# Kernel tuning notes

Hardware: AMD Instinct MI355X
Metric: run time of the kernel (lower is better)

Reference implementation:

```python
import jax, jax.numpy as jnp
import numpy as np

# Surrogate-gradient spike (ActFun_adp from DH-SNN): Heaviside fwd, multi-Gaussian bwd
GAMMA, LENS, SCALE, HIGHT = 0.5, 0.5, 6.0, 0.15
VTH = 1.0

def _gauss(x, mu, sigma):
    return jnp.exp(-((x - mu) ** 2) / (2.0 * sigma ** 2)) / (jnp.sqrt(2.0 * jnp.pi) * sigma)

@jax.custom_vjp
def spike_fn(x):
    return (x > 0).astype(x.dtype)

def _spike_fwd(x):
    return spike_fn(x), x

def _spike_bwd(x, g):
    temp = (_gauss(x, 0.0, LENS) * (1.0 + HIGHT)
            - _gauss(x, LENS, SCALE * LENS) * HIGHT
            - _gauss(x, -LENS, SCALE * LENS) * HIGHT)
    return (g * temp * GAMMA,)

spike_fn.defvjp(_spike_fwd, _spike_bwd)

B, T, IN, H, OUT = 128, 1000, 700, 512, 20

def setup_inputs() -> dict:
    key = jax.random.key(0)
    ks = jax.random.split(key, 10)
    lim1 = float(1.0 / np.sqrt(IN))
    lim2 = float(1.0 / np.sqrt(H))
    return {
        "x": jax.random.uniform(ks[0], (B, T, IN), jnp.float32),
        "W1": jax.random.uniform(ks[1], (H, IN), jnp.float32, -lim1, lim1),
        "b1": jax.random.uniform(ks[2], (H,), jnp.float32, -lim1, lim1),
        "tau_m1": jax.random.uniform(ks[3], (H,), jnp.float32, 0.0, 4.0),
        "tau_n1": jax.random.uniform(ks[4], (H,), jnp.float32, 0.0, 4.0),
        "W2": jax.random.uniform(ks[5], (OUT, H), jnp.float32, -lim2, lim2),
        "b2": jax.random.uniform(ks[6], (OUT,), jnp.float32, -lim2, lim2),
        "tau_m2": jax.random.uniform(ks[7], (OUT,), jnp.float32, 0.0, 4.0),
        "mem1_0": jax.random.uniform(ks[8], (B, H), jnp.float32),   # set_neuron_state uses rand init
        "mem2_0": jax.random.uniform(ks[9], (B, OUT), jnp.float32),
    }

def reference(x, W1, b1, tau_m1, tau_n1, W2, b2, tau_m2, mem1_0, mem2_0):
    alpha1 = jax.nn.sigmoid(tau_m1)   # [H] membrane decay
    beta1 = jax.nn.sigmoid(tau_n1)    # [H] dendritic decay (branch=1 -> branch dim collapsed)
    alpha2 = jax.nn.sigmoid(tau_m2)   # [OUT] readout decay
    # Input projection is time-invariant: one big GEMM instead of T small ones.
    proj = jnp.einsum('bti,hi->bth', x, W1) + b1  # [B,T,H]

    def step(carry, p_t):
        mem1, spike1, d_in, mem2 = carry
        d_in = beta1 * d_in + (1.0 - beta1) * p_t                       # dendritic filter
        mem1 = mem1 * alpha1 + (1.0 - alpha1) * d_in - VTH * spike1      # LIF soft reset
        spike1 = spike_fn(mem1 - VTH)
        mem2 = mem2 * alpha2 + (1.0 - alpha2) * (spike1 @ W2.T + b2)     # leaky readout
        return (mem1, spike1, d_in, mem2), mem2

    init = (mem1_0, jnp.zeros_like(mem1_0), jnp.zeros_like(mem1_0), mem2_0)
    _, outs = jax.lax.scan(step, init, jnp.swapaxes(proj, 0, 1))  # scan over time
    return jnp.swapaxes(outs, 0, 1)  # [B, T, OUT]
```

## Files before the change

kernel.cpp:

```cpp
#include <hip/hip_runtime.h>
#include <stdint.h>

#define Bd   128
#define Td   1000
#define INd  700
#define Hd   512
#define OUTd 20
#define Md   (Bd * Td)
#define KPAD 704
#define KIT  22
#define KH   1408

typedef _Float16 f16;
typedef f16 f16x4 __attribute__((ext_vector_type(4)));
typedef f16 f16x8 __attribute__((ext_vector_type(8)));
typedef float f32x4 __attribute__((ext_vector_type(4)));

__device__ __forceinline__ void gld_lds16(const void* g, void* l) {
  __builtin_amdgcn_global_load_lds(
      (__attribute__((address_space(1))) void*)(g),
      (__attribute__((address_space(3))) void*)(l), 16, 0, 0);
}

__global__ __launch_bounds__(256) void pack_kernel(
    const float* __restrict__ src, f16* __restrict__ dst, int nrows) {
  const int t = blockIdx.x * 256 + threadIdx.x;
  if (t >= nrows * 88) return;
  const int m = t / 88;
  const int rem = t - m * 88;
  const int kt = rem >> 2;
  const int lc = rem & 3;
  const int k0 = kt * 32 + lc * 8;
  const float* sp = src + (size_t)m * INd + k0;
  float v[8];
  if (k0 + 8 <= INd) {
    const float4 v0 = *(const float4*)sp;
    const float4 v1 = *(const float4*)(sp + 4);
    v[0] = v0.x; v[1] = v0.y; v[2] = v0.z; v[3] = v0.w;
    v[4] = v1.x; v[5] = v1.y; v[6] = v1.z; v[7] = v1.w;
  } else {
#pragma unroll
    for (int u = 0; u < 8; ++u) v[u] = (k0 + u < INd) ? sp[u] : 0.f;
  }
  f16x8 h1, h2;
#pragma unroll
  for (int u = 0; u < 8; ++u) {
    const f16 a = (f16)v[u];
    h1[u] = a;
    h2[u] = (f16)(v[u] - (float)a);
  }
  const int s = m & 7;
  f16* out = dst + (size_t)m * KH + (size_t)kt * 64;
  *(f16x8*)(out + ((lc ^ s) << 3)) = h1;
  *(f16x8*)(out + (((lc + 4) ^ s) << 3)) = h2;
}

__global__ __launch_bounds__(512) void gemm1_kernel(
    const f16* __restrict__ Xp, const f16* __restrict__ Wp,
    const float* __restrict__ b1, float* __restrict__ proj) {
  __shared__ __align__(16) f16 As[2][256 * 64];
  __shared__ __align__(16) f16 Bs[2][256 * 64];
  const int tid = threadIdx.x;

  const int l = blockIdx.x;
  const int bb = (l & 7) * 125 + (l >> 3);
  const int m0 = (bb >> 1) << 8;
  const int n0 = (bb & 1) << 8;

  const int srow = tid >> 3, sc = tid & 7;
  const f16* Ag = Xp + (size_t)(m0 + srow) * KH + (sc << 3);
  const f16* Bg = Wp + (size_t)(n0 + srow) * KH + (sc << 3);

  const int wv = tid >> 6, lane = tid & 63;
  const int wm0 = (wv >> 2) << 7;
  const int wn0 = (wv & 3) << 6;
  const int fr = lane & 15;
  const int fq = lane >> 4;
  const int swz = (fr & 7) << 4;
  const int o1 = ((fq << 4) ^ swz) >> 1;
  const int o2 = (((fq + 4) << 4) ^ swz) >> 1;

  f32x4 acc[8][4];
#pragma unroll
  for (int i = 0; i < 8; ++i)
#pragma unroll
    for (int j = 0; j < 4; ++j) acc[i][j] = (f32x4){0.f, 0.f, 0.f, 0.f};

#pragma unroll
  for (int j = 0; j < 4; ++j) {
    gld_lds16(Ag + (size_t)j * (64 * KH), &As[0][tid * 8 + j * 4096]);
    gld_lds16(Bg + (size_t)j * (64 * KH), &Bs[0][tid * 8 + j * 4096]);
  }

#pragma unroll 1
  for (int t = 0; t < KIT; ++t) {
    asm volatile("s_waitcnt vmcnt(0)" ::: "memory");
    __builtin_amdgcn_sched_barrier(0);
    __builtin_amdgcn_s_barrier();

    const f16* Ac = As[t & 1];
    const f16* Bc = Bs[t & 1];
    const int nb = (t & 1) ^ 1;
    const bool pf = (t + 1 < KIT);
    const size_t go = (size_t)(t + 1) << 6;

#pragma unroll
    for (int ph = 0; ph < 4; ++ph) {
      const int mh = ph >> 1, nh = ph & 1;
      f16x8 a1f[4], a2f[4], b1f[2], b2f[2];
#pragma unroll
      for (int mi = 0; mi < 4; ++mi) {
        const int rb = (wm0 + mh * 64 + mi * 16 + fr) << 6;
        a1f[mi] = *(const f16x8*)&Ac[rb + o1];
        a2f[mi] = *(const f16x8*)&Ac[rb + o2];
      }
#pragma unroll
      for (int nj = 0; nj < 2; ++nj) {
        const int cb = (wn0 + nh * 32 + nj * 16 + fr) << 6;
        b1f[nj] = *(const f16x8*)&Bc[cb + o1];
        b2f[nj] = *(const f16x8*)&Bc[cb + o2];
      }
      if (pf && ph == 0) {
#pragma unroll
        for (int j = 0; j < 4; ++j)
          gld_lds16(Ag + (size_t)j * (64 * KH) + go,
                    &As[nb][tid * 8 + j * 4096]);
      }
      if (pf && ph == 1) {
#pragma unroll
        for (int j = 0; j < 4; ++j)
          gld_lds16(Bg + (size_t)j * (64 * KH) + go,
                    &Bs[nb][tid * 8 + j * 4096]);
      }
      __builtin_amdgcn_sched_barrier(0);
      __builtin_amdgcn_s_barrier();
      asm volatile("s_waitcnt lgkmcnt(0)" ::: "memory");
      __builtin_amdgcn_sched_barrier(0);
      __builtin_amdgcn_s_setprio(1);
#pragma unroll
      for (int mi = 0; mi < 4; ++mi)
#pragma unroll
        for (int nj = 0; nj < 2; ++nj) {
          f32x4 a = acc[(mh << 2) + mi][(nh << 1) + nj];
          a = __builtin_amdgcn_mfma_f32_16x16x32_f16(a1f[mi], b1f[nj], a, 0, 0, 0);
          a = __builtin_amdgcn_mfma_f32_16x16x32_f16(a1f[mi], b2f[nj], a, 0, 0, 0);
          a = __builtin_amdgcn_mfma_f32_16x16x32_f16(a2f[mi], b1f[nj], a, 0, 0, 0);
          acc[(mh << 2) + mi][(nh << 1) + nj] = a;
        }
      __builtin_amdgcn_s_setprio(0);
      __builtin_amdgcn_sched_barrier(0);
      __builtin_amdgcn_s_barrier();
    }
  }

#pragma unroll
  for (int ni = 0; ni < 4; ++ni) {
    const int n = n0 + wn0 + ni * 16 + fr;
    const float bias = b1[n];
#pragma unroll
    for (int mi = 0; mi < 8; ++mi) {
      const int mb = m0 + wm0 + mi * 16 + (fq << 2);
      float* p = proj + (size_t)mb * Hd + n;
#pragma unroll
      for (int rr = 0; rr < 4; ++rr)
        p[(size_t)rr * Hd] = acc[mi][ni][rr] + bias;
    }
  }
}

__global__ __launch_bounds__(256) void w1split_kernel(
    const float* __restrict__ W1, f16* __restrict__ W1a,
    f16* __restrict__ W1b) {
  const int idx = blockIdx.x * 256 + threadIdx.x;
  if (idx >= 512 * KPAD) return;
  const int n = idx / KPAD, k = idx - n * KPAD;
  const float v = (k < INd) ? W1[n * INd + k] : 0.f;
  const f16 h1 = (f16)v;
  const f16 h2 = (f16)(v - (float)h1);
  W1a[idx] = h1;
  W1b[idx] = h2;
}

__global__ __launch_bounds__(256) void gemm1_fb_kernel(
    const float* __restrict__ X, const f16* __restrict__ W1a,
    const f16* __restrict__ W1b, const float* __restrict__ b1,
    float* __restrict__ proj) {
  __shared__ __align__(16) f16 A1s[128 * 40];
  __shared__ __align__(16) f16 A2s[128 * 40];
  __shared__ __align__(16) f16 B1s[128 * 40];
  __shared__ __align__(16) f16 B2s[128 * 40];

  const int tid = threadIdx.x;
  const int n0 = blockIdx.x * 128;
  const int m0 = blockIdx.y * 128;

  const int srow = tid >> 1;
  const int skq  = (tid & 1) << 4;

  const float* Xp  = X + (size_t)(m0 + srow) * INd;
  const f16*   Bap = W1a + (size_t)(n0 + srow) * KPAD + skq;
  const f16*   Bbp = W1b + (size_t)(n0 + srow) * KPAD + skq;

  const int wv = tid >> 6, lane = tid & 63;
  const int wm0 = (wv >> 1) * 64, wn0 = (wv & 1) * 64;
  const int fr = lane & 15;
  const int fq = lane >> 4;

  f32x4 acc[4][4];
#pragma unroll
  for (int i = 0; i < 4; ++i)
#pragma unroll
    for (int j = 0; j < 4; ++j) acc[i][j] = (f32x4){0.f, 0.f, 0.f, 0.f};

  const float4 z4 = make_float4(0.f, 0.f, 0.f, 0.f);
  float4 ax[4];
  f16x8 bq1[2], bq2[2];

#pragma unroll
  for (int i = 0; i < 4; ++i) ax[i] = *(const float4*)(Xp + skq + 4 * i);
  bq1[0] = *(const f16x8*)(Bap);     bq1[1] = *(const f16x8*)(Bap + 8);
  bq2[0] = *(const f16x8*)(Bbp);     bq2[1] = *(const f16x8*)(Bbp + 8);

#pragma unroll 1
  for (int it = 0; it < KIT; ++it) {
    __syncthreads();
#pragma unroll
    for (int i = 0; i < 4; ++i) {
      const float4 v = ax[i];
      f16x4 h1, h2;
      h1.x = (f16)v.x; h2.x = (f16)(v.x - (float)h1.x);
      h1.y = (f16)v.y; h2.y = (f16)(v.y - (float)h1.y);
      h1.z = (f16)v.z; h2.z = (f16)(v.z - (float)h1.z);
      h1.w = (f16)v.w; h2.w = (f16)(v.w - (float)h1.w);
      *(f16x4*)&A1s[srow * 40 + skq + 4 * i] = h1;
      *(f16x4*)&A2s[srow * 40 + skq + 4 * i] = h2;
    }
    *(f16x8*)&B1s[srow * 40 + skq]     = bq1[0];
    *(f16x8*)&B1s[srow * 40 + skq + 8] = bq1[1];
    *(f16x8*)&B2s[srow * 40 + skq]     = bq2[0];
    *(f16x8*)&B2s[srow * 40 + skq + 8] = bq2[1];
    __syncthreads();
    if (it + 1 < KIT) {
      const int k0 = (it + 1) * 32;
#pragma unroll
      for (int i = 0; i < 4; ++i) {
        const int k = k0 + skq + 4 * i;
        ax[i] = (k + 4 <= INd) ? *(const float4*)(Xp + k) : z4;
      }
      bq1[0] = *(const f16x8*)(Bap + k0);
      bq1[1] = *(const f16x8*)(Bap + k0 + 8);
      bq2[0] = *(const f16x8*)(Bbp + k0);
      bq2[1] = *(const f16x8*)(Bbp + k0 + 8);
    }
    f16x8 a1f[4], a2f[4], b1f[4], b2f[4];
#pragma unroll
    for (int mi = 0; mi < 4; ++mi) {
      const int off = (wm0 + mi * 16 + fr) * 40 + fq * 8;
      a1f[mi] = *(const f16x8*)&A1s[off];
      a2f[mi] = *(const f16x8*)&A2s[off];
    }
#pragma unroll
    for (int ni = 0; ni < 4; ++ni) {
      const int off = (wn0 + ni * 16 + fr) * 40 + fq * 8;
      b1f[ni] = *(const f16x8*)&B1s[off];
      b2f[ni] = *(const f16x8*)&B2s[off];
    }
#pragma unroll
    for (int mi = 0; mi < 4; ++mi)
#pragma unroll
      for (int ni = 0; ni < 4; ++ni) {
        acc[mi][ni] = __builtin_amdgcn_mfma_f32_16x16x32_f16(
            a1f[mi], b1f[ni], acc[mi][ni], 0, 0, 0);
        acc[mi][ni] = __builtin_amdgcn_mfma_f32_16x16x32_f16(
            a1f[mi], b2f[ni], acc[mi][ni], 0, 0, 0);
        acc[mi][ni] = __builtin_amdgcn_mfma_f32_16x16x32_f16(
            a2f[mi], b1f[ni], acc[mi][ni], 0, 0, 0);
      }
  }

#pragma unroll
  for (int ni = 0; ni < 4; ++ni) {
    const int n = n0 + wn0 + ni * 16 + fr;
    const float bias = b1[n];
#pragma unroll
    for (int mi = 0; mi < 4; ++mi) {
      const int mb = m0 + wm0 + mi * 16 + fq * 4;
      float* p = proj + (size_t)mb * Hd + n;
#pragma unroll
      for (int r = 0; r < 4; ++r)
        p[(size_t)r * Hd] = acc[mi][ni][r] + bias;
    }
  }
}

#define S1_PHASE(QC, QN, T0)                                      \
  {                                                               \
    const int tp_ = (T0) + 24;                                    \
    _Pragma("unroll")                                             \
    for (int u = 0; u < 8; ++u) {                                 \
      const int tt = (tp_ + u < Td) ? (tp_ + u) : (Td - 1);       \
      buf[QN][u] = pp[(size_t)tt * Hd];                           \
    }                                                             \
    _Pragma("unroll")                                             \
    for (int u = 0; u < 8; ++u) {                                 \
      const float pv = buf[QC][u];                                \
      d = bn * d + ombn * pv;                                     \
      mem = am * mem + omam * d - s;                              \
      const bool fire = mem > 1.0f;                               \
      s = fire ? 1.f : 0.f;                                       \
      const unsigned long long msk = __ballot(fire);              \
      if (lane == 0) sp[(size_t)((T0) + u) * 8] = msk;            \
    }                                                             \
  }

__global__ __launch_bounds__(256) void scan1_kernel(
    const float* __restrict__ proj, const float* __restrict__ tau_m1,
    const float* __restrict__ tau_n1, const float* __restrict__ mem1_0,
    unsigned long long* __restrict__ spk) {
  const int gid = blockIdx.x * 256 + threadIdx.x;
  const int b = gid >> 9;
  const int h = gid & 511;
  const float am = 1.f / (1.f + expf(-tau_m1[h]));
  const float bn = 1.f / (1.f + expf(-tau_n1[h]));
  const float omam = 1.f - am, ombn = 1.f - bn;
  float mem = mem1_0[(b << 9) | h];
  float d = 0.f, s = 0.f;
  const float* pp = proj + (size_t)b * Td * Hd + h;
  unsigned long long* sp = spk + (size_t)b * Td * 8 + (h >> 6);
  const int lane = threadIdx.x & 63;

  float buf[4][8];
#pragma unroll
  for (int q = 0; q < 3; ++q)
#pragma unroll
    for (int u = 0; u < 8; ++u)
      buf[q][u] = pp[(size_t)(q * 8 + u) * Hd];

#pragma unroll 1
  for (int t0 = 0; t0 < 992; t0 += 32) {
    S1_PHASE(0, 3, t0);
    S1_PHASE(1, 0, t0 + 8);
    S1_PHASE(2, 1, t0 + 16);
    S1_PHASE(3, 2, t0 + 24);
  }
  S1_PHASE(0, 3, 992);
}

__global__ __launch_bounds__(256) void gemm2_kernel(
    const unsigned long long* __restrict__ spk, const float* __restrict__ W2,
    const float* __restrict__ b2, float* __restrict__ R, int Mtotal) {
  __shared__ float W2s[Hd * OUTd];
  const int tid = threadIdx.x;
  for (int idx = tid; idx < Hd * OUTd; idx += 256) {
    const int h = idx / OUTd, o = idx - h * OUTd;
    W2s[idx] = W2[o * Hd + h];
  }
  __syncthreads();
  const int wave = tid >> 6, lane = tid & 63;
  const int mg = lane / OUTd;
  const int o = lane - mg * OUTd;
  if (mg >= 3) return;
  const float bias = b2[o];
  const int mbase = blockIdx.x * 96 + wave * 24 + mg;
#pragma unroll 1
  for (int i = 0; i < 8; ++i) {
    const int m = mbase + i * 3;
    if (m >= Mtotal) break;
    float r = bias;
    const unsigned long long* mp = spk + (size_t)m * 8;
#pragma unroll
    for (int c = 0; c < 8; ++c) {
      unsigned long long mask = mp[c];
      const float* wrow = W2s + (c << 6) * OUTd + o;
      while (mask) {
        const int j = __builtin_ctzll(mask);
        mask &= mask - 1;
        r += wrow[j * OUTd];
      }
    }
    R[(size_t)m * OUTd + o] = r;
  }
}

__global__ __launch_bounds__(256) void scan2_kernel(
    const float* __restrict__ R, const float* __restrict__ tau_m2,
    const float* __restrict__ mem2_0, float* __restrict__ out) {
  __shared__ float leS[8][20];
  __shared__ float stS[8][20];
  const int b = blockIdx.x;
  const int tid = threadIdx.x;
  const int c = tid / OUTd;
  const int o = tid - c * OUTd;
  const bool active = tid < 160;
  float a2 = 0.f, oma2 = 0.f;
  if (active) {
    a2 = 1.f / (1.f + expf(-tau_m2[o]));
    oma2 = 1.f - a2;
  }
  const float* Rb = R + (size_t)b * Td * OUTd;
  float* Ob = out + (size_t)b * Td * OUTd;
  const int t0 = c * 125;

  if (active) {
    float m = 0.f;
    for (int u = 0; u < 125; ++u)
      m = a2 * m + oma2 * Rb[(size_t)(t0 + u) * OUTd + o];
    leS[c][o] = m;
  }
  __syncthreads();
  if (tid < OUTd) {
    const float a = 1.f / (1.f + expf(-tau_m2[tid]));
    float aL = 1.f;
    for (int i = 0; i < 125; ++i) aL *= a;
    float m = mem2_0[b * OUTd + tid];
    for (int cc = 0; cc < 8; ++cc) {
      stS[cc][tid] = m;
      m = aL * m + leS[cc][tid];
    }
  }
  __syncthreads();
  if (active) {
    float m = stS[c][o];
    for (int u = 0; u < 125; ++u) {
      m = a2 * m + oma2 * Rb[(size_t)(t0 + u) * OUTd + o];
      Ob[(size_t)(t0 + u) * OUTd + o] = m;
    }
  }
}

extern "C" void kernel_launch(void* const* d_in, const int* in_sizes, int n_in,
                              void* d_out, int out_size, void* d_ws, size_t ws_size,
                              hipStream_t stream) {
  const float* x      = (const float*)d_in[0];
  const float* W1     = (const float*)d_in[1];
  const float* b1     = (const float*)d_in[2];
  const float* tau_m1 = (const float*)d_in[3];
  const float* tau_n1 = (const float*)d_in[4];
  const float* W2     = (const float*)d_in[5];
  const float* b2     = (const float*)d_in[6];
  const float* tau_m2 = (const float*)d_in[7];
  const float* mem1_0 = (const float*)d_in[8];
  const float* mem2_0 = (const float*)d_in[9];
  float* out = (float*)d_out;

  const size_t proj_b = (size_t)Md * Hd * sizeof(float);
  const size_t xp_b   = (size_t)Md * KH * sizeof(f16);
  const size_t wp_b   = (size_t)512 * KH * sizeof(f16);
  const size_t spk_b  = (size_t)Md * 8 * sizeof(unsigned long long);

  float* proj = (float*)d_ws;

  if (ws_size >= proj_b + xp_b + wp_b) {
    f16* Xpk = (f16*)((char*)d_ws + proj_b);
    f16* Wpk = (f16*)((char*)d_ws + proj_b + xp_b);
    unsigned long long* spk = (unsigned long long*)((char*)d_ws + proj_b);
    float* R = (float*)((char*)d_ws + proj_b + spk_b);

    pack_kernel<<<dim3(Md * 88 / 256), 256, 0, stream>>>(x, Xpk, Md);
    pack_kernel<<<dim3(512 * 88 / 256), 256, 0, stream>>>(W1, Wpk, 512);
    gemm1_kernel<<<dim3((Hd / 256) * (Md / 256)), 512, 0, stream>>>(Xpk, Wpk,
                                                                    b1, proj);
    scan1_kernel<<<dim3(Bd * Hd / 256), 256, 0, stream>>>(proj, tau_m1, tau_n1,
                                                          mem1_0, spk);
    gemm2_kernel<<<dim3((Md + 95) / 96), 256, 0, stream>>>(spk, W2, b2, R, Md);
    scan2_kernel<<<dim3(Bd), 256, 0, stream>>>(R, tau_m2, mem2_0, out);
  } else {
    unsigned long long* spk =
        (unsigned long long*)((char*)d_ws + proj_b);
    float* R = (float*)((char*)spk + spk_b);
    f16* W1a = (f16*)R;
    f16* W1b = W1a + 512 * KPAD;

    w1split_kernel<<<dim3((512 * KPAD + 255) / 256), 256, 0, stream>>>(W1, W1a,
                                                                       W1b);
    gemm1_fb_kernel<<<dim3(Hd / 128, Md / 128), 256, 0, stream>>>(x, W1a, W1b,
                                                                  b1, proj);
    scan1_kernel<<<dim3(Bd * Hd / 256), 256, 0, stream>>>(proj, tau_m1, tau_n1,
                                                          mem1_0, spk);
    gemm2_kernel<<<dim3((Md + 95) / 96), 256, 0, stream>>>(spk, W2, b2, R, Md);
    scan2_kernel<<<dim3(Bd), 256, 0, stream>>>(R, tau_m2, mem2_0, out);
  }
}
```

Baseline: 970.0 us.

## Software-pipeline LDS fragment loads with MFMA phases using ping-pong registers

Restructures the GEMM1 inner loop so each phase's LDS fragment reads are issued while the previous phase's MFMAs run, using two register fragment sets (even/odd). The per-phase block barriers and lgkmcnt waits are removed, leaving one barrier per K-iteration, and the next tile's first fragments are prefetched before the last MFMA phase. The launch bounds also now request 2 blocks per CU. This costs extra VGPRs for the duplicated fragments. Requesting higher occupancy at 512 threads may force spills, and the LDS footprint may not fit two blocks anyway.

```diff
diff --git a/kernel.cpp b/kernel.cpp
--- a/kernel.cpp
+++ b/kernel.cpp
@@ -55,7 +55,47 @@
   *(f16x8*)(out + (((lc + 4) ^ s) << 3)) = h2;
 }
 
-__global__ __launch_bounds__(512) void gemm1_kernel(
+#define SBAR __builtin_amdgcn_sched_barrier(0)
+
+#define LOAD_FRAGS(S, MH, NH, AB, BB)                                   \
+  _Pragma("unroll")                                                     \
+  for (int mi = 0; mi < 4; ++mi) {                                      \
+    const int rb = (wm0 + (MH) * 64 + mi * 16 + fr) << 6;               \
+    a1##S[mi] = *(const f16x8*)&(AB)[rb + o1];                          \
+    a2##S[mi] = *(const f16x8*)&(AB)[rb + o2];                          \
+  }                                                                     \
+  _Pragma("unroll")                                                     \
+  for (int nj = 0; nj < 2; ++nj) {                                      \
+    const int cb = (wn0 + (NH) * 32 + nj * 16 + fr) << 6;               \
+    b1##S[nj] = *(const f16x8*)&(BB)[cb + o1];                          \
+    b2##S[nj] = *(const f16x8*)&(BB)[cb + o2];                          \
+  }
+
+#define MFMA_PHASE(S, MH, NH)                                           \
+  __builtin_amdgcn_s_setprio(1);                                        \
+  _Pragma("unroll")                                                     \
+  for (int mi = 0; mi < 4; ++mi)                                        \
+  _Pragma("unroll")                                                     \
+  for (int nj = 0; nj < 2; ++nj) {                                      \
+    f32x4 a = acc[(MH) * 4 + mi][(NH) * 2 + nj];                        \
+    a = __builtin_amdgcn_mfma_f32_16x16x32_f16(a1##S[mi], b1##S[nj], a, 0, 0, 0); \
+    a = __builtin_amdgcn_mfma_f32_16x16x32_f16(a1##S[mi], b2##S[nj], a, 0, 0, 0); \
+    a = __builtin_amdgcn_mfma_f32_16x16x32_f16(a2##S[mi], b1##S[nj], a, 0, 0, 0); \
+    acc[(MH) * 4 + mi][(NH) * 2 + nj] = a;                              \
+  }                                                                     \
+  __builtin_amdgcn_s_setprio(0);
+
+#define STAGE_A(NB, GO)                                                 \
+  _Pragma("unroll")                                                     \
+  for (int j = 0; j < 4; ++j)                                           \
+    gld_lds16(Ag + (size_t)j * (64 * KH) + (GO), &As[NB][tid * 8 + j * 4096]);
+
+#define STAGE_B(NB, GO)                                                 \
+  _Pragma("unroll")                                                     \
+  for (int j = 0; j < 4; ++j)                                           \
+    gld_lds16(Bg + (size_t)j * (64 * KH) + (GO), &Bs[NB][tid * 8 + j * 4096]);
+
+__global__ __launch_bounds__(512, 2) void gemm1_kernel(
     const f16* __restrict__ Xp, const f16* __restrict__ Wp,
     const float* __restrict__ b1, float* __restrict__ proj) {
   __shared__ __align__(16) f16 As[2][256 * 64];
@@ -86,71 +126,47 @@
 #pragma unroll
     for (int j = 0; j < 4; ++j) acc[i][j] = (f32x4){0.f, 0.f, 0.f, 0.f};
 
-#pragma unroll
-  for (int j = 0; j < 4; ++j) {
-    gld_lds16(Ag + (size_t)j * (64 * KH), &As[0][tid * 8 + j * 4096]);
-    gld_lds16(Bg + (size_t)j * (64 * KH), &Bs[0][tid * 8 + j * 4096]);
-  }
+  f16x8 a1E[4], a2E[4], b1E[2], b2E[2];
+  f16x8 a1O[4], a2O[4], b1O[2], b2O[2];
+
+  STAGE_A(0, 0);
+  STAGE_B(0, 0);
+  asm volatile("s_waitcnt vmcnt(0)" ::: "memory");
+  __builtin_amdgcn_sched_barrier(0);
+  __builtin_amdgcn_s_barrier();
+  LOAD_FRAGS(E, 0, 0, As[0], Bs[0]);
 
 #pragma unroll 1
   for (int t = 0; t < KIT; ++t) {
-    asm volatile("s_waitcnt vmcnt(0)" ::: "memory");
-    __builtin_amdgcn_sched_barrier(0);
-    __builtin_amdgcn_s_barrier();
-
     const f16* Ac = As[t & 1];
     const f16* Bc = Bs[t & 1];
     const int nb = (t & 1) ^ 1;
     const bool pf = (t + 1 < KIT);
     const size_t go = (size_t)(t + 1) << 6;
 
-#pragma unroll
-    for (int ph = 0; ph < 4; ++ph) {
-      const int mh = ph >> 1, nh = ph & 1;
-      f16x8 a1f[4], a2f[4], b1f[2], b2f[2];
-#pragma unroll
-      for (int mi = 0; mi < 4; ++mi) {
-        const int rb = (wm0 + mh * 64 + mi * 16 + fr) << 6;
-        a1f[mi] = *(const f16x8*)&Ac[rb + o1];
-        a2f[mi] = *(const f16x8*)&Ac[rb + o2];
-      }
-#pragma unroll
-      for (int nj = 0; nj < 2; ++nj) {
-        const int cb = (wn0 + nh * 32 + nj * 16 + fr) << 6;
-        b1f[nj] = *(const f16x8*)&Bc[cb + o1];
-        b2f[nj] = *(const f16x8*)&Bc[cb + o2];
-      }
-      if (pf && ph == 0) {
-#pragma unroll
-        for (int j = 0; j < 4; ++j)
-          gld_lds16(Ag + (size_t)j * (64 * KH) + go,
-                    &As[nb][tid * 8 + j * 4096]);
-      }
-      if (pf && ph == 1) {
-#pragma unroll
-        for (int j = 0; j < 4; ++j)
-          gld_lds16(Bg + (size_t)j * (64 * KH) + go,
-                    &Bs[nb][tid * 8 + j * 4096]);
-      }
+    LOAD_FRAGS(O, 0, 1, Ac, Bc);
+    if (pf) { STAGE_A(nb, go); }
+    SBAR;
+    MFMA_PHASE(E, 0, 0);
+    SBAR;
+    LOAD_FRAGS(E, 1, 0, Ac, Bc);
+    if (pf) { STAGE_B(nb, go); }
+    SBAR;
+    MFMA_PHASE(O, 0, 1);
+    SBAR;
+    LOAD_FRAGS(O, 1, 1, Ac, Bc);
+    SBAR;
+    MFMA_PHASE(E, 1, 0);
+    SBAR;
+    if (pf) {
+      asm volatile("s_waitcnt vmcnt(0) lgkmcnt(0)" ::: "memory");
       __builtin_amdgcn_sched_barrier(0);
       __builtin_amdgcn_s_barrier();
-      asm volatile("s_waitcnt lgkmcnt(0)" ::: "memory");
-      __builtin_amdgcn_sched_barrier(0);
-      __builtin_amdgcn_s_setprio(1);
-#pragma unroll
-      for (int mi = 0; mi < 4; ++mi)
-#pragma unroll
-        for (int nj = 0; nj < 2; ++nj) {
-          f32x4 a = acc[(mh << 2) + mi][(nh << 1) + nj];
-          a = __builtin_amdgcn_mfma_f32_16x16x32_f16(a1f[mi], b1f[nj], a, 0, 0, 0);
-          a = __builtin_amdgcn_mfma_f32_16x16x32_f16(a1f[mi], b2f[nj], a, 0, 0, 0);
-          a = __builtin_amdgcn_mfma_f32_16x16x32_f16(a2f[mi], b1f[nj], a, 0, 0, 0);
-          acc[(mh << 2) + mi][(nh << 1) + nj] = a;
-        }
-      __builtin_amdgcn_s_setprio(0);
-      __builtin_amdgcn_sched_barrier(0);
-      __builtin_amdgcn_s_barrier();
-    }
+      LOAD_FRAGS(E, 0, 0, As[nb], Bs[nb]);
+    }
+    SBAR;
+    MFMA_PHASE(O, 1, 1);
+    SBAR;
   }
 
 #pragma unroll
```

Measured after the change: 926.6 us. 4.5% less time.
